# Optimization experiments

Measured on AMD Instinct MI355X. Metric: run time of the kernel, lower is better.

Reference implementation:

```python
import jax, jax.numpy as jnp
import numpy as np

V, MAXLEN, D, I, C, L, S = 32000, 4096, 1024, 4096, 1024, 4, 4096


def setup_inputs() -> dict:
    key = jax.random.key(0)
    ks = jax.random.split(key, 20)
    sd = 0.02
    inp = {
        "input_indices": jax.random.randint(ks[0], (S,), 0, V),
        "emb": jax.random.normal(ks[1], (V, D), jnp.float32) * sd,
        "pos": jax.random.normal(ks[2], (MAXLEN, D), jnp.float32) * sd,
        "Wq": jax.random.normal(ks[3], (L, D, I), jnp.float32) * sd,
        "bq": jnp.zeros((L, I), jnp.float32),
        "Wk": jax.random.normal(ks[4], (L, D, I), jnp.float32) * sd,
        "bk": jnp.zeros((L, I), jnp.float32),
        "Wv": jax.random.normal(ks[5], (L, D, I), jnp.float32) * sd,
        "bv": jnp.zeros((L, I), jnp.float32),
        "Wo": jax.random.normal(ks[6], (L, I, D), jnp.float32) * sd,
        "bo": jnp.zeros((L, D), jnp.float32),
        "W1": jax.random.normal(ks[7], (L, D, I), jnp.float32) * sd,
        "b1": jnp.zeros((L, I), jnp.float32),
        "W2": jax.random.normal(ks[8], (L, I, D), jnp.float32) * sd,
        "b2": jnp.zeros((L, D), jnp.float32),
        "Wout": jax.random.normal(ks[9], (D, C), jnp.float32) * sd,
        "bout": jnp.zeros((C,), jnp.float32),
    }
    return inp


def reference(input_indices, emb, pos, Wq, bq, Wk, bk, Wv, bv, Wo, bo, W1, b1, W2, b2, Wout, bout):
    s = input_indices.shape[0]
    x = emb[input_indices] + pos[:s]  # [S, D]
    causal_mask = jnp.triu(jnp.ones((s, s), bool), k=1)  # True above diagonal -> masked
    scale = 1.0 / np.sqrt(Wq.shape[-1]).astype(np.float32)

    def layer(x, p):
        wq, bq_, wk, bk_, wv, bv_, wo, bo_, w1, b1_, w2, b2_ = p
        q = x @ wq + bq_  # [S, I]
        k = x @ wk + bk_
        v = x @ wv + bv_
        scores = (q @ k.T) * scale  # [S, S]
        scores = jnp.where(causal_mask, -jnp.inf, scores)
        attn = jax.nn.softmax(scores, axis=-1)
        r = x + (attn @ v) @ wo + bo_  # residual + attention output projection
        f = jnp.maximum(r @ w1 + b1_, 0.0) @ w2 + b2_  # ReLU FFN
        return r + f, attn

    x, attention_maps = jax.lax.scan(
        layer, x, (Wq, bq, Wk, bk, Wv, bv, Wo, bo, W1, b1, W2, b2)
    )
    logits = x @ Wout + bout  # [S, C]
    log_probs = jax.nn.log_softmax(logits, axis=-1)
    return log_probs, attention_maps  # [S, C], [L, S, S]
```

## Files before the change

kernel.cpp:

```cpp
#include <hip/hip_runtime.h>
#include <stdint.h>
#include <math.h>

#define S_ 4096
#define D_ 1024
#define I_ 4096
#define C_ 1024
#define L_ 4

typedef unsigned short u16;
typedef short bf16x8 __attribute__((ext_vector_type(8)));
typedef float f32x4 __attribute__((ext_vector_type(4)));

__device__ __forceinline__ u16 f2bf(float f) {
  union { float f; uint32_t u; } c; c.f = f;
  return (u16)((c.u + 0x7FFFu + ((c.u >> 16) & 1u)) >> 16);
}

__device__ __forceinline__ u16 f2h(float f) {
  _Float16 h = (_Float16)f;
  return *(u16*)&h;
}
__device__ __forceinline__ float h2f(u16 b) {
  _Float16 h = *(_Float16*)&b;
  return (float)h;
}

__device__ __forceinline__ void gll16(const void* g, void* l) {
  __builtin_amdgcn_global_load_lds(
      (__attribute__((address_space(1))) void*)(g),
      (__attribute__((address_space(3))) void*)(l), 16, 0, 0);
}

#define BAR() asm volatile("s_barrier" ::: "memory")
#define WAITV(n) asm volatile("s_waitcnt vmcnt(" #n ")" ::: "memory")

__device__ __forceinline__ int xcd_swz(int orig, int nwg) {
  int q8 = nwg >> 3, r8 = nwg & 7;
  int xcd = orig & 7, rem = orig >> 3;
  return (xcd < r8 ? xcd * (q8 + 1) : r8 * (q8 + 1) + (xcd - r8) * q8) + rem;
}

__device__ __forceinline__ void gemm256_body(
    u16* sA, u16* sB,
    const u16* __restrict__ A, const u16* __restrict__ Bt,
    const float* __restrict__ bias, const float* __restrict__ resid,
    float* __restrict__ outF, u16* __restrict__ outB, u16* __restrict__ outH,
    int N, int K, float scale, int relu,
    int row0, int col0, int t0, int t1)
{
  int tid = threadIdx.x, l = tid & 63;
  int w = tid >> 6;
  int wr = w >> 2, wc = w & 3;
  int lrow = l & 15, lq = l >> 4;
  int hb = wc >> 1;
  int rx = lrow & 7;

  const u16* ap[2]; const u16* bp[2]; int dst[2];
#pragma unroll
  for (int u = 0; u < 2; ++u) {
    int c = u * 512 + tid;
    int row = c >> 3;
    int oct = (c & 7) ^ (row & 7);
    ap[u] = A + (size_t)(row0 + row) * K + oct * 8;
    bp[u] = Bt + (size_t)(col0 + row) * K + oct * 8;
    dst[u] = c * 8;
  }

#define STAGE_A(par, hh, t)                                                     \
  { _Pragma("unroll") for (int u = 0; u < 2; ++u)                               \
      gll16(ap[u] + (size_t)(hh) * 128 * K + (t) * 64,                          \
            &sA[((par) * 2 + (hh)) * 8192 + dst[u]]); }
#define STAGE_B(par, hh, t)                                                     \
  { _Pragma("unroll") for (int u = 0; u < 2; ++u)                               \
      gll16(bp[u] + (size_t)(hh) * 128 * K + (t) * 64,                          \
            &sB[((par) * 2 + (hh)) * 8192 + dst[u]]); }
#define LD_A(DST, par, mh)                                                      \
  { _Pragma("unroll") for (int mi = 0; mi < 4; ++mi)                            \
    _Pragma("unroll") for (int kc = 0; kc < 2; ++kc)                            \
      DST[mi][kc] = *(const bf16x8*)&sA[((par) * 2 + wr) * 8192 +               \
          ((mh) * 64 + mi * 16 + lrow) * 64 + (((kc * 4 + lq) ^ rx) * 8)]; }
#define LD_B(DST, par, nh)                                                      \
  { _Pragma("unroll") for (int nj = 0; nj < 2; ++nj)                            \
    _Pragma("unroll") for (int kc = 0; kc < 2; ++kc)                            \
      DST[nj][kc] = *(const bf16x8*)&sB[((par) * 2 + hb) * 8192 +               \
          ((wc & 1) * 64 + (nh) * 32 + nj * 16 + lrow) * 64 +                   \
          (((kc * 4 + lq) ^ rx) * 8)]; }

  f32x4 acc[8][4];
#pragma unroll
  for (int i = 0; i < 8; ++i)
#pragma unroll
    for (int j = 0; j < 4; ++j) {
      acc[i][j][0] = 0.f; acc[i][j][1] = 0.f; acc[i][j][2] = 0.f; acc[i][j][3] = 0.f;
    }

#define MM(AF, MB, NB)                                                          \
  { __builtin_amdgcn_s_setprio(1);                                             \
    _Pragma("unroll") for (int kc = 0; kc < 2; ++kc)                            \
    _Pragma("unroll") for (int mi = 0; mi < 4; ++mi)                            \
    _Pragma("unroll") for (int nj = 0; nj < 2; ++nj)                            \
      acc[(MB) + mi][(NB) + nj] = __builtin_amdgcn_mfma_f32_16x16x32_bf16(      \
          AF[mi][kc], bfv[nj][kc], acc[(MB) + mi][(NB) + nj], 0, 0, 0);         \
    __builtin_amdgcn_s_setprio(0); }

  bf16x8 afA[4][2], afB[4][2], bfv[2][2];

  STAGE_A(0, 0, t0); STAGE_A(0, 1, t0); STAGE_B(0, 0, t0); STAGE_B(0, 1, t0);
  STAGE_A(1, 0, t0 + 1); STAGE_A(1, 1, t0 + 1); STAGE_B(1, 0, t0 + 1);
  WAITV(6);
  BAR();

  for (int t = t0; t < t1; ++t) {
    int p = (t - t0) & 1;
    LD_A(afA, p, 0);
    LD_B(bfv, p, 0);
    LD_A(afB, p, 1);
    if (t + 1 < t1) STAGE_B(p ^ 1, 1, t + 1);
    BAR();
    MM(afA, 0, 0);
    BAR();
    if (t + 2 < t1) STAGE_A(p, 0, t + 2);
    BAR();
    MM(afB, 4, 0);
    BAR();
    LD_B(bfv, p, 1);
    if (t + 2 < t1) STAGE_A(p, 1, t + 2);
    BAR();
    MM(afB, 4, 2);
    BAR();
    if (t + 2 < t1) STAGE_B(p, 0, t + 2);
    BAR();
    MM(afA, 0, 2);
    if (t + 2 < t1) { WAITV(6); } else { WAITV(0); }
    BAR();
  }
#undef STAGE_A
#undef STAGE_B
#undef LD_A
#undef LD_B
#undef MM

  float biasv[4] = {0.f, 0.f, 0.f, 0.f};
  if (bias) {
#pragma unroll
    for (int j = 0; j < 4; ++j) biasv[j] = bias[col0 + wc * 64 + j * 16 + lrow];
  }
#pragma unroll
  for (int i = 0; i < 8; ++i) {
#pragma unroll
    for (int r = 0; r < 4; ++r) {
      int row = row0 + wr * 128 + i * 16 + lq * 4 + r;
      size_t ro = (size_t)row * N;
#pragma unroll
      for (int j = 0; j < 4; ++j) {
        int col = col0 + wc * 64 + j * 16 + lrow;
        float v = acc[i][j][r] * scale + biasv[j];
        if (resid) v += resid[ro + col];
        if (relu) v = fmaxf(v, 0.f);
        if (outF) outF[ro + col] = v;
        if (outB) outB[ro + col] = f2bf(v);
        if (outH) outH[ro + col] = f2h(v);
      }
    }
  }
}

__global__ __launch_bounds__(512, 2) void gemm256k(
    const u16* __restrict__ A, const u16* __restrict__ Bt,
    const float* __restrict__ bias, const float* __restrict__ resid,
    float* __restrict__ outF, u16* __restrict__ outB,
    int M, int N, int K, float scale, int flags, int k0, int k1)
{
  extern __shared__ char smem[];
  int wg = xcd_swz(blockIdx.x, gridDim.x);
  int nbx = N / 256;
  int br = wg / nbx, bc = wg % nbx;
  gemm256_body((u16*)smem, (u16*)smem + 32768, A, Bt, bias, resid, outF, outB,
               nullptr, N, K, scale, flags & 1, br * 256, bc * 256,
               k0 / 64, k1 / 64);
}

struct B3 { const float* b[3]; };
__global__ __launch_bounds__(512, 2) void gemm256_qkv(
    const u16* __restrict__ A, const u16* __restrict__ BtBase,
    B3 b3, u16* __restrict__ outBase, int K)
{
  extern __shared__ char smem[];
  int wg = xcd_swz(blockIdx.x, gridDim.x);
  int z = wg >> 8;
  int tile = wg & 255;
  int br = tile >> 4, bc = tile & 15;
  gemm256_body((u16*)smem, (u16*)smem + 32768, A,
               BtBase + (size_t)z * I_ * D_, b3.b[z], nullptr,
               nullptr, outBase + (size_t)z * S_ * I_, nullptr,
               I_, K, 1.0f, 0, br * 256, bc * 256, 0, K / 64);
}

__global__ __launch_bounds__(512, 2) void gemm256_tri3(
    const u16* __restrict__ A, const u16* __restrict__ Bt,
    u16* __restrict__ out0, u16* __restrict__ out1, u16* __restrict__ out2,
    int K, float scale)
{
  extern __shared__ char smem[];
  int wg = xcd_swz(blockIdx.x, gridDim.x);
  int ntri = gridDim.x / 3;
  int chunk = wg / ntri;
  int tile = wg - chunk * ntri;
  int br = (int)((sqrtf(8.0f * (float)tile + 1.0f) - 1.0f) * 0.5f);
  while ((br + 1) * (br + 2) / 2 <= tile) ++br;
  while (br * (br + 1) / 2 > tile) --br;
  int bc = tile - br * (br + 1) / 2;
  int t0 = (chunk == 0) ? 0 : (chunk == 1 ? 22 : 43);
  int t1 = (chunk == 0) ? 22 : (chunk == 1 ? 43 : 64);
  u16* o = (chunk == 0) ? out0 : (chunk == 1 ? out1 : out2);
  gemm256_body((u16*)smem, (u16*)smem + 32768, A, Bt, nullptr, nullptr,
               nullptr, nullptr, o, S_, K, scale, 0, br * 256, bc * 256, t0, t1);
}

__global__ __launch_bounds__(512, 2) void gemm256_pv(
    const u16* __restrict__ A, const u16* __restrict__ Bt,
    u16* __restrict__ outB, u16* __restrict__ pvH)
{
  extern __shared__ char smem[];
  int wg = xcd_swz(blockIdx.x, gridDim.x);
  if (wg < 128) {
    int br = wg >> 4, bc = wg & 15;
    gemm256_body((u16*)smem, (u16*)smem + 32768, A, Bt, nullptr, nullptr,
                 nullptr, outB, nullptr, I_, S_, 1.0f, 0,
                 br * 256, bc * 256, 0, (br + 1) * 4);
  } else {
    int c = wg - 128;
    int br = 8 + (c >> 5);
    int bc = (c >> 1) & 15;
    int chunk = c & 1;
    int lim = (br + 1) * 4;
    int half = lim >> 1;
    u16* o = pvH + (size_t)chunk * (S_ / 2) * I_ - (size_t)2048 * I_;
    gemm256_body((u16*)smem, (u16*)smem + 32768, A, Bt, nullptr, nullptr,
                 nullptr, nullptr, o, I_, S_, 1.0f, 0,
                 br * 256, bc * 256, chunk ? half : 0, chunk ? lim : half);
  }
}

__global__ __launch_bounds__(256) void combine2pv(
    const u16* __restrict__ pvH, u16* __restrict__ outB)
{
  const int MN = (S_ / 2) * I_;
  int i = (blockIdx.x * 256 + threadIdx.x) * 4;
  ushort4 a = *(const ushort4*)&pvH[i];
  ushort4 b = *(const ushort4*)&pvH[MN + i];
  ushort4 o;
  o.x = f2bf(h2f(a.x) + h2f(b.x));
  o.y = f2bf(h2f(a.y) + h2f(b.y));
  o.z = f2bf(h2f(a.z) + h2f(b.z));
  o.w = f2bf(h2f(a.w) + h2f(b.w));
  *(ushort4*)&outB[(size_t)2048 * I_ + i] = o;
}

__global__ __launch_bounds__(512, 2) void gemm256_ks4(
    const u16* __restrict__ A, const u16* __restrict__ Bt,
    u16* __restrict__ pOut, int M, int N, int K)
{
  extern __shared__ char smem[];
  int wg = xcd_swz(blockIdx.x, gridDim.x);
  int chunk = wg & 3;
  int tile = wg >> 2;
  int nbx = N / 256;
  int br = tile / nbx, bc = tile % nbx;
  u16* o = pOut + (size_t)chunk * M * N;
  int kq = K / 4;
  gemm256_body((u16*)smem, (u16*)smem + 32768, A, Bt, nullptr, nullptr,
               nullptr, nullptr, o, N, K, 1.0f, 0,
               br * 256, bc * 256, (chunk * kq) / 64, ((chunk + 1) * kq) / 64);
}

__global__ __launch_bounds__(256) void combine4(
    const u16* __restrict__ p, const float* __restrict__ bias,
    const float* __restrict__ resid, float* __restrict__ outF,
    u16* __restrict__ outB, int MN, int N)
{
  int i = (blockIdx.x * 256 + threadIdx.x) * 4;
  ushort4 a = *(const ushort4*)&p[i];
  ushort4 b = *(const ushort4*)&p[MN + i];
  ushort4 c = *(const ushort4*)&p[2 * MN + i];
  ushort4 d = *(const ushort4*)&p[3 * MN + i];
  f32x4 v;
  v[0] = h2f(a.x) + h2f(b.x) + h2f(c.x) + h2f(d.x);
  v[1] = h2f(a.y) + h2f(b.y) + h2f(c.y) + h2f(d.y);
  v[2] = h2f(a.z) + h2f(b.z) + h2f(c.z) + h2f(d.z);
  v[3] = h2f(a.w) + h2f(b.w) + h2f(c.w) + h2f(d.w);
  int col = i & (N - 1);
  v += *(const f32x4*)&bias[col];
  v += *(const f32x4*)&resid[i];
  *(f32x4*)&outF[i] = v;
  ushort4 o;
  o.x = f2bf(v[0]); o.y = f2bf(v[1]); o.z = f2bf(v[2]); o.w = f2bf(v[3]);
  *(ushort4*)&outB[i] = o;
}

template <int BM_, int BN_>
__global__ __launch_bounds__(256) void gemm_bt(
    const u16* __restrict__ A, const u16* __restrict__ Bt,
    const float* __restrict__ bias, const float* __restrict__ resid,
    float* __restrict__ outF, u16* __restrict__ outB,
    int M, int N, int K, float scale, int flags)
{
  constexpr int FM = BM_ / 32;
  constexpr int FN = BN_ / 32;
  constexpr int ALOADS = BM_ * 8 / 256;
  constexpr int BLOADS = BN_ * 8 / 256;
  constexpr int WROWS = BM_ / 2;
  constexpr int WCOLS = BN_ / 2;

  int wg = xcd_swz(blockIdx.x, gridDim.x);
  int nbx = N / BN_;
  int br = wg / nbx, bc = wg % nbx;

  int tid = threadIdx.x;
  int l = tid & 63, w = tid >> 6;
  int wr = w >> 1, wc = w & 1;
  int lrow = l & 15, lq = l >> 4;
  int row0 = br * BM_, col0 = bc * BN_;

  __shared__ u16 lA[2][BM_ * 64];
  __shared__ u16 lB[2][BN_ * 64];

  const u16* aptr[ALOADS];
  const u16* bptr[BLOADS];
#pragma unroll
  for (int t = 0; t < ALOADS; ++t) {
    int c = t * 256 + tid;
    int row = c >> 3;
    int oct = (c & 7) ^ (row & 7);
    aptr[t] = A + (size_t)(row0 + row) * K + oct * 8;
  }
#pragma unroll
  for (int t = 0; t < BLOADS; ++t) {
    int c = t * 256 + tid;
    int row = c >> 3;
    int oct = (c & 7) ^ (row & 7);
    bptr[t] = Bt + (size_t)(col0 + row) * K + oct * 8;
  }

#define STAGE(b, koff)                                                          \
  {                                                                             \
    _Pragma("unroll") for (int t = 0; t < ALOADS; ++t)                          \
        gll16(aptr[t] + (koff), &lA[b][(t * 256 + tid) * 8]);                   \
    _Pragma("unroll") for (int t = 0; t < BLOADS; ++t)                          \
        gll16(bptr[t] + (koff), &lB[b][(t * 256 + tid) * 8]);                   \
  }

  f32x4 acc[FM][FN];
#pragma unroll
  for (int i = 0; i < FM; ++i)
#pragma unroll
    for (int j = 0; j < FN; ++j) {
      acc[i][j][0] = 0.f; acc[i][j][1] = 0.f; acc[i][j][2] = 0.f; acc[i][j][3] = 0.f;
    }

  int ktiles = K / 64;
  int rxA = lrow & 7;

  STAGE(0, 0);
  __syncthreads();
  int cur = 0;
  for (int kt = 0; kt < ktiles; ++kt) {
    if (kt + 1 < ktiles) STAGE(cur ^ 1, (kt + 1) * 64);
#pragma unroll
    for (int kc = 0; kc < 2; ++kc) {
      int kq = kc * 4 + lq;
      int octA = (kq ^ rxA) * 8;
      bf16x8 af[FM], bfv[FN];
#pragma unroll
      for (int i = 0; i < FM; ++i)
        af[i] = *(const bf16x8*)&lA[cur][(wr * WROWS + i * 16 + lrow) * 64 + octA];
#pragma unroll
      for (int j = 0; j < FN; ++j)
        bfv[j] = *(const bf16x8*)&lB[cur][(wc * WCOLS + j * 16 + lrow) * 64 + octA];
#pragma unroll
      for (int i = 0; i < FM; ++i)
#pragma unroll
        for (int j = 0; j < FN; ++j)
          acc[i][j] = __builtin_amdgcn_mfma_f32_16x16x32_bf16(af[i], bfv[j], acc[i][j], 0, 0, 0);
    }
    __syncthreads();
    cur ^= 1;
  }
#undef STAGE

  float biasv[FN];
#pragma unroll
  for (int j = 0; j < FN; ++j) biasv[j] = 0.f;
  if (bias) {
#pragma unroll
    for (int j = 0; j < FN; ++j) biasv[j] = bias[col0 + wc * WCOLS + j * 16 + lrow];
  }
  bool do_relu = (flags & 1) != 0;
#pragma unroll
  for (int i = 0; i < FM; ++i) {
#pragma unroll
    for (int r = 0; r < 4; ++r) {
      int row = row0 + wr * WROWS + i * 16 + lq * 4 + r;
      size_t ro = (size_t)row * N;
#pragma unroll
      for (int j = 0; j < FN; ++j) {
        int col = col0 + wc * WCOLS + j * 16 + lrow;
        float v = acc[i][j][r] * scale + biasv[j];
        if (resid) v += resid[ro + col];
        if (do_relu) v = fmaxf(v, 0.f);
        if (outF) outF[ro + col] = v;
        if (outB) outB[ro + col] = f2bf(v);
      }
    }
  }
}

struct T6 {
  const float* src[6];
  u16* dst[6];
};

__global__ __launch_bounds__(256) void trans6_f2b(T6 a) {
  __shared__ float tile[32][33];
  int z = blockIdx.z;
  bool big = (z == 3 || z == 5);
  int R = big ? I_ : D_;
  int C = big ? D_ : I_;
  int bid = blockIdx.y * gridDim.x + blockIdx.x;
  int nbx = C / 32;
  int bx = bid % nbx, by = bid / nbx;
  const float* src = a.src[z];
  u16* dst = a.dst[z];
  int c0 = bx * 32, r0 = by * 32;
  int tx = threadIdx.x & 31, ty = threadIdx.x >> 5;
#pragma unroll
  for (int i = 0; i < 32; i += 8)
    tile[ty + i][tx] = src[(size_t)(r0 + ty + i) * C + c0 + tx];
  __syncthreads();
#pragma unroll
  for (int i = 0; i < 32; i += 8)
    dst[(size_t)(c0 + ty + i) * R + r0 + tx] = f2bf(tile[tx][ty + i]);
}

__global__ __launch_bounds__(256) void trans_f2b(const float* __restrict__ src,
                                                 u16* __restrict__ dst, int R, int C)
{
  __shared__ float tile[32][33];
  int c0 = blockIdx.x * 32, r0 = blockIdx.y * 32;
  int tx = threadIdx.x & 31, ty = threadIdx.x >> 5;
#pragma unroll
  for (int i = 0; i < 32; i += 8)
    tile[ty + i][tx] = src[(size_t)(r0 + ty + i) * C + c0 + tx];
  __syncthreads();
#pragma unroll
  for (int i = 0; i < 32; i += 8)
    dst[(size_t)(c0 + ty + i) * R + r0 + tx] = f2bf(tile[tx][ty + i]);
}

__global__ __launch_bounds__(256) void trans_b2b(const u16* __restrict__ src,
                                                 u16* __restrict__ dst, int R, int C)
{
  __shared__ u16 tile[64][68];
  int c0 = blockIdx.x * 64, r0 = blockIdx.y * 64;
  int tx = threadIdx.x & 63, ty = threadIdx.x >> 6;
#pragma unroll
  for (int i = 0; i < 64; i += 4)
    tile[ty + i][tx] = src[(size_t)(r0 + ty + i) * C + c0 + tx];
  __syncthreads();
#pragma unroll
  for (int i = 0; i < 64; i += 4)
    dst[(size_t)(c0 + ty + i) * R + r0 + tx] = tile[tx][ty + i];
}

__global__ __launch_bounds__(256) void embed_k(const int* __restrict__ idx,
                                               const float* __restrict__ emb,
                                               const float* __restrict__ pos,
                                               float* __restrict__ xf, u16* __restrict__ xb)
{
  int s = blockIdx.y;
  int d = blockIdx.x * 256 + threadIdx.x;
  float v = emb[(size_t)idx[s] * D_ + d] + pos[(size_t)s * D_ + d];
  size_t o = (size_t)s * D_ + d;
  xf[o] = v;
  xb[o] = f2bf(v);
}

__global__ __launch_bounds__(256) void softmax_causal(float* __restrict__ att,
                                                      const u16* __restrict__ p0,
                                                      const u16* __restrict__ p1,
                                                      const u16* __restrict__ p2,
                                                      u16* __restrict__ attB)
{
  int s = blockIdx.x;
  __shared__ float row[S_];
  __shared__ float red[8];
  int tid = threadIdx.x, l = tid & 63, w = tid >> 6;
  int nv = s + 1;
  size_t base = (size_t)s * S_;
  float m = -3.0e38f;
  for (int c = tid; c < nv; c += 256) {
    float v = h2f(p0[base + c]) + h2f(p1[base + c]) + h2f(p2[base + c]);
    row[c] = v; m = fmaxf(m, v);
  }
#pragma unroll
  for (int off = 32; off; off >>= 1) m = fmaxf(m, __shfl_xor(m, off, 64));
  if (l == 0) red[w] = m;
  __syncthreads();
  m = fmaxf(fmaxf(red[0], red[1]), fmaxf(red[2], red[3]));
  float sum = 0.f;
  for (int c = tid; c < nv; c += 256) { float e = __expf(row[c] - m); row[c] = e; sum += e; }
#pragma unroll
  for (int off = 32; off; off >>= 1) sum += __shfl_xor(sum, off, 64);
  if (l == 0) red[4 + w] = sum;
  __syncthreads();
  sum = red[4] + red[5] + red[6] + red[7];
  float inv = 1.0f / sum;
  int nb = ((s >> 8) + 1) * 256;
  for (int c = tid; c < S_; c += 256) {
    float p = (c < nv) ? row[c] * inv : 0.0f;
    att[base + c] = p;
    if (c < nb) attB[base + c] = f2bf(p);
  }
}

__global__ __launch_bounds__(256) void logsoftmax_k(const float* __restrict__ logits,
                                                    float* __restrict__ out)
{
  int s = blockIdx.x;
  int tid = threadIdx.x, l = tid & 63, w = tid >> 6;
  __shared__ float red[8];
  size_t base = (size_t)s * C_;
  float v[4];
  float m = -3.0e38f;
#pragma unroll
  for (int k = 0; k < 4; ++k) { v[k] = logits[base + tid + k * 256]; m = fmaxf(m, v[k]); }
#pragma unroll
  for (int off = 32; off; off >>= 1) m = fmaxf(m, __shfl_xor(m, off, 64));
  if (l == 0) red[w] = m;
  __syncthreads();
  m = fmaxf(fmaxf(red[0], red[1]), fmaxf(red[2], red[3]));
  float sum = 0.f;
#pragma unroll
  for (int k = 0; k < 4; ++k) sum += __expf(v[k] - m);
#pragma unroll
  for (int off = 32; off; off >>= 1) sum += __shfl_xor(sum, off, 64);
  if (l == 0) red[4 + w] = sum;
  __syncthreads();
  sum = red[4] + red[5] + red[6] + red[7];
  float lz = logf(sum);
#pragma unroll
  for (int k = 0; k < 4; ++k) out[base + tid + k * 256] = v[k] - m - lz;
}

extern "C" void kernel_launch(void* const* d_in, const int* in_sizes, int n_in,
                              void* d_out, int out_size, void* d_ws, size_t ws_size,
                              hipStream_t stream) {
  (void)in_sizes; (void)n_in; (void)out_size; (void)ws_size;
  const int*   idx  = (const int*)d_in[0];
  const float* emb  = (const float*)d_in[1];
  const float* pos  = (const float*)d_in[2];
  const float* Wq   = (const float*)d_in[3];
  const float* bq   = (const float*)d_in[4];
  const float* Wk   = (const float*)d_in[5];
  const float* bk   = (const float*)d_in[6];
  const float* Wv   = (const float*)d_in[7];
  const float* bv   = (const float*)d_in[8];
  const float* Wo   = (const float*)d_in[9];
  const float* bo   = (const float*)d_in[10];
  const float* W1   = (const float*)d_in[11];
  const float* b1   = (const float*)d_in[12];
  const float* W2   = (const float*)d_in[13];
  const float* b2   = (const float*)d_in[14];
  const float* Wout = (const float*)d_in[15];
  const float* bout = (const float*)d_in[16];
  float* out = (float*)d_out;

  char* ws = (char*)d_ws;
  const size_t MB = 1024ull * 1024ull;
  float* xres  = (float*)(ws + 0);
  u16*  xbf    = (u16*)(ws + 16 * MB);
  u16*  bufQ   = (u16*)(ws + 24 * MB);
  u16*  bufK   = (u16*)(ws + 56 * MB);
  u16*  bufV   = (u16*)(ws + 88 * MB);
  u16*  bufVT  = (u16*)(ws + 120 * MB);
  u16*  attnB  = (u16*)(ws + 152 * MB);
  float* logit = (float*)(ws + 184 * MB);
  u16* WqT   = (u16*)(ws + 200 * MB);
  u16* WkT   = (u16*)(ws + 208 * MB);
  u16* WvT   = (u16*)(ws + 216 * MB);
  u16* WoT   = (u16*)(ws + 224 * MB);
  u16* W1T   = (u16*)(ws + 232 * MB);
  u16* W2T   = (u16*)(ws + 240 * MB);
  u16* WoutT = (u16*)(ws + 248 * MB);
  u16* attP0 = (u16*)(ws + 256 * MB);
  u16* attP1 = (u16*)(ws + 288 * MB);
  u16* attP2 = (u16*)(ws + 320 * MB);
  u16* shP   = (u16*)(ws + 352 * MB);

  const float iscale = 1.0f / 64.0f;
  const int LDSB = 131072;
  hipFuncSetAttribute((const void*)gemm256k,
                      hipFuncAttributeMaxDynamicSharedMemorySize, LDSB);
  hipFuncSetAttribute((const void*)gemm256_qkv,
                      hipFuncAttributeMaxDynamicSharedMemorySize, LDSB);
  hipFuncSetAttribute((const void*)gemm256_tri3,
                      hipFuncAttributeMaxDynamicSharedMemorySize, LDSB);
  hipFuncSetAttribute((const void*)gemm256_pv,
                      hipFuncAttributeMaxDynamicSharedMemorySize, LDSB);
  hipFuncSetAttribute((const void*)gemm256_ks4,
                      hipFuncAttributeMaxDynamicSharedMemorySize, LDSB);
  const int G_SQ = (S_ / 256) * (I_ / 256);

  embed_k<<<dim3(D_ / 256, S_), 256, 0, stream>>>(idx, emb, pos, xres, xbf);

  for (int layer = 0; layer < L_; ++layer) {
    T6 t6;
    t6.src[0] = Wq + (size_t)layer * D_ * I_; t6.dst[0] = WqT;
    t6.src[1] = Wk + (size_t)layer * D_ * I_; t6.dst[1] = WkT;
    t6.src[2] = Wv + (size_t)layer * D_ * I_; t6.dst[2] = WvT;
    t6.src[3] = Wo + (size_t)layer * I_ * D_; t6.dst[3] = WoT;
    t6.src[4] = W1 + (size_t)layer * D_ * I_; t6.dst[4] = W1T;
    t6.src[5] = W2 + (size_t)layer * I_ * D_; t6.dst[5] = W2T;
    trans6_f2b<<<dim3(128, 32, 6), 256, 0, stream>>>(t6);

    B3 b3;
    b3.b[0] = bq + (size_t)layer * I_;
    b3.b[1] = bk + (size_t)layer * I_;
    b3.b[2] = bv + (size_t)layer * I_;
    gemm256_qkv<<<3 * G_SQ, 512, LDSB, stream>>>(xbf, WqT, b3, bufQ, D_);

    trans_b2b<<<dim3(I_ / 64, S_ / 64), 256, 0, stream>>>(bufV, bufVT, S_, I_);

    float* attL = out + (size_t)S_ * C_ + (size_t)layer * S_ * S_;
    gemm256_tri3<<<3 * 136, 512, LDSB, stream>>>(bufQ, bufK, attP0, attP1, attP2,
                                                 I_, iscale);

    softmax_causal<<<S_, 256, 0, stream>>>(attL, attP0, attP1, attP2, attnB);

    gemm256_pv<<<384, 512, LDSB, stream>>>(attnB, bufVT, bufQ, shP);
    combine2pv<<<(S_ / 2) * (I_ / 1024), 256, 0, stream>>>(shP, bufQ);

    gemm256_ks4<<<(S_ / 256) * (D_ / 256) * 4, 512, LDSB, stream>>>(
        bufQ, WoT, shP, S_, D_, I_);
    combine4<<<(S_ * D_) / 1024, 256, 0, stream>>>(
        shP, bo + (size_t)layer * D_, xres, xres, xbf, S_ * D_, D_);

    gemm256k<<<G_SQ, 512, LDSB, stream>>>(
        xbf, W1T, b1 + (size_t)layer * I_, nullptr, nullptr, bufK,
        S_, I_, D_, 1.0f, 1, 0, D_);

    gemm256_ks4<<<(S_ / 256) * (D_ / 256) * 4, 512, LDSB, stream>>>(
        bufK, W2T, shP, S_, D_, I_);
    combine4<<<(S_ * D_) / 1024, 256, 0, stream>>>(
        shP, b2 + (size_t)layer * D_, xres, xres, xbf, S_ * D_, D_);
  }

  trans_f2b<<<dim3(C_ / 32, D_ / 32), 256, 0, stream>>>(Wout, WoutT, D_, C_);
  gemm_bt<64, 128><<<(S_ / 64) * (C_ / 128), 256, 0, stream>>>(
      xbf, WoutT, bout, nullptr, logit, nullptr, S_, C_, D_, 1.0f, 0);
  logsoftmax_k<<<S_, 256, 0, stream>>>(logit, out);
}
```

Measured before the change: 2.181 ms.

## Write V transposed from QKV GEMM epilogue, widen weight transpose and embed tiles

The QKV GEMM now writes the V projection straight into the transposed layout the PV GEMM needs, staging each half of the output tile through LDS. This removes the separate bf16 transpose kernel and its extra pass over the 32 MB V buffer. The weight transpose kernel moves to 64x64 tiles and the embedding kernel is vectorised to handle 8 elements per thread. The transposed epilogue adds two barriers and an LDS round trip to the V tiles, and its LDS layout with a row pitch of 264 may cause bank conflicts.

Measured after the change: 2.214 ms. About the same (+1.5%).

```diff
diff --git a/kernel.cpp b/kernel.cpp
--- a/kernel.cpp
+++ b/kernel.cpp
@@ -46,6 +46,7 @@
     const u16* __restrict__ A, const u16* __restrict__ Bt,
     const float* __restrict__ bias, const float* __restrict__ resid,
     float* __restrict__ outF, u16* __restrict__ outB, u16* __restrict__ outH,
+    u16* __restrict__ outT, int ldT,
     int N, int K, float scale, int relu,
     int row0, int col0, int t0, int t1)
 {
@@ -146,6 +147,37 @@
 #pragma unroll
     for (int j = 0; j < 4; ++j) biasv[j] = bias[col0 + wc * 64 + j * 16 + lrow];
   }
+
+  if (outT) {
+    u16* tlds = sA;
+    int myhalf = wc >> 1;
+#pragma unroll
+    for (int half = 0; half < 2; ++half) {
+      BAR();
+      if (myhalf == half) {
+#pragma unroll
+        for (int i = 0; i < 8; ++i)
+#pragma unroll
+          for (int r = 0; r < 4; ++r)
+#pragma unroll
+            for (int j = 0; j < 4; ++j) {
+              int cl = (wc * 64 + j * 16 + lrow) & 127;
+              int rowl = wr * 128 + i * 16 + lq * 4 + r;
+              tlds[cl * 264 + rowl] = f2bf(acc[i][j][r] + biasv[j]);
+            }
+      }
+      BAR();
+      int cl = tid >> 2, seg = tid & 3;
+      size_t gb = (size_t)(col0 + half * 128 + cl) * ldT + row0 + seg * 64;
+#pragma unroll
+      for (int r8 = 0; r8 < 64; r8 += 8) {
+        bf16x8 v = *(const bf16x8*)&tlds[cl * 264 + seg * 64 + r8];
+        *(bf16x8*)&outT[gb + r8] = v;
+      }
+    }
+    return;
+  }
+
 #pragma unroll
   for (int i = 0; i < 8; ++i) {
 #pragma unroll
@@ -177,24 +209,31 @@
   int nbx = N / 256;
   int br = wg / nbx, bc = wg % nbx;
   gemm256_body((u16*)smem, (u16*)smem + 32768, A, Bt, bias, resid, outF, outB,
-               nullptr, N, K, scale, flags & 1, br * 256, bc * 256,
+               nullptr, nullptr, 0, N, K, scale, flags & 1, br * 256, bc * 256,
                k0 / 64, k1 / 64);
 }
 
 struct B3 { const float* b[3]; };
 __global__ __launch_bounds__(512, 2) void gemm256_qkv(
     const u16* __restrict__ A, const u16* __restrict__ BtBase,
-    B3 b3, u16* __restrict__ outBase, int K)
+    B3 b3, u16* __restrict__ outQK, u16* __restrict__ vT, int K)
 {
   extern __shared__ char smem[];
   int wg = xcd_swz(blockIdx.x, gridDim.x);
   int z = wg >> 8;
   int tile = wg & 255;
   int br = tile >> 4, bc = tile & 15;
-  gemm256_body((u16*)smem, (u16*)smem + 32768, A,
-               BtBase + (size_t)z * I_ * D_, b3.b[z], nullptr,
-               nullptr, outBase + (size_t)z * S_ * I_, nullptr,
-               I_, K, 1.0f, 0, br * 256, bc * 256, 0, K / 64);
+  if (z < 2) {
+    gemm256_body((u16*)smem, (u16*)smem + 32768, A,
+                 BtBase + (size_t)z * I_ * D_, b3.b[z], nullptr,
+                 nullptr, outQK + (size_t)z * S_ * I_, nullptr, nullptr, 0,
+                 I_, K, 1.0f, 0, br * 256, bc * 256, 0, K / 64);
+  } else {
+    gemm256_body((u16*)smem, (u16*)smem + 32768, A,
+                 BtBase + (size_t)2 * I_ * D_, b3.b[2], nullptr,
+                 nullptr, nullptr, nullptr, vT, S_,
+                 I_, K, 1.0f, 0, br * 256, bc * 256, 0, K / 64);
+  }
 }
 
 __global__ __launch_bounds__(512, 2) void gemm256_tri3(
@@ -215,7 +254,8 @@
   int t1 = (chunk == 0) ? 22 : (chunk == 1 ? 43 : 64);
   u16* o = (chunk == 0) ? out0 : (chunk == 1 ? out1 : out2);
   gemm256_body((u16*)smem, (u16*)smem + 32768, A, Bt, nullptr, nullptr,
-               nullptr, nullptr, o, S_, K, scale, 0, br * 256, bc * 256, t0, t1);
+               nullptr, nullptr, o, nullptr, 0,
+               S_, K, scale, 0, br * 256, bc * 256, t0, t1);
 }
 
 __global__ __launch_bounds__(512, 2) void gemm256_pv(
@@ -227,7 +267,7 @@
   if (wg < 128) {
     int br = wg >> 4, bc = wg & 15;
     gemm256_body((u16*)smem, (u16*)smem + 32768, A, Bt, nullptr, nullptr,
-                 nullptr, outB, nullptr, I_, S_, 1.0f, 0,
+                 nullptr, outB, nullptr, nullptr, 0, I_, S_, 1.0f, 0,
                  br * 256, bc * 256, 0, (br + 1) * 4);
   } else {
     int c = wg - 128;
@@ -238,7 +278,7 @@
     int half = lim >> 1;
     u16* o = pvH + (size_t)chunk * (S_ / 2) * I_ - (size_t)2048 * I_;
     gemm256_body((u16*)smem, (u16*)smem + 32768, A, Bt, nullptr, nullptr,
-                 nullptr, nullptr, o, I_, S_, 1.0f, 0,
+                 nullptr, nullptr, o, nullptr, 0, I_, S_, 1.0f, 0,
                  br * 256, bc * 256, chunk ? half : 0, chunk ? lim : half);
   }
 }
@@ -271,7 +311,7 @@
   u16* o = pOut + (size_t)chunk * M * N;
   int kq = K / 4;
   gemm256_body((u16*)smem, (u16*)smem + 32768, A, Bt, nullptr, nullptr,
-               nullptr, nullptr, o, N, K, 1.0f, 0,
+               nullptr, nullptr, o, nullptr, 0, N, K, 1.0f, 0,
                br * 256, bc * 256, (chunk * kq) / 64, ((chunk + 1) * kq) / 64);
 }
 
@@ -422,17 +462,32 @@
 };
 
 __global__ __launch_bounds__(256) void trans6_f2b(T6 a) {
-  __shared__ float tile[32][33];
+  __shared__ float tile[64][65];
   int z = blockIdx.z;
   bool big = (z == 3 || z == 5);
   int R = big ? I_ : D_;
   int C = big ? D_ : I_;
   int bid = blockIdx.y * gridDim.x + blockIdx.x;
-  int nbx = C / 32;
+  int nbx = C / 64;
   int bx = bid % nbx, by = bid / nbx;
   const float* src = a.src[z];
   u16* dst = a.dst[z];
-  int c0 = bx * 32, r0 = by * 32;
+  int c0 = bx * 64, r0 = by * 64;
+  int tx = threadIdx.x & 63, ty = threadIdx.x >> 6;
+#pragma unroll
+  for (int i = 0; i < 64; i += 4)
+    tile[ty + i][tx] = src[(size_t)(r0 + ty + i) * C + c0 + tx];
+  __syncthreads();
+#pragma unroll
+  for (int i = 0; i < 64; i += 4)
+    dst[(size_t)(c0 + ty + i) * R + r0 + tx] = f2bf(tile[tx][ty + i]);
+}
+
+__global__ __launch_bounds__(256) void trans_f2b(const float* __restrict__ src,
+                                                 u16* __restrict__ dst, int R, int C)
+{
+  __shared__ float tile[32][33];
+  int c0 = blockIdx.x * 32, r0 = blockIdx.y * 32;
   int tx = threadIdx.x & 31, ty = threadIdx.x >> 5;
 #pragma unroll
   for (int i = 0; i < 32; i += 8)
@@ -441,36 +496,6 @@
 #pragma unroll
   for (int i = 0; i < 32; i += 8)
     dst[(size_t)(c0 + ty + i) * R + r0 + tx] = f2bf(tile[tx][ty + i]);
-}
-
-__global__ __launch_bounds__(256) void trans_f2b(const float* __restrict__ src,
-                                                 u16* __restrict__ dst, int R, int C)
-{
-  __shared__ float tile[32][33];
-  int c0 = blockIdx.x * 32, r0 = blockIdx.y * 32;
-  int tx = threadIdx.x & 31, ty = threadIdx.x >> 5;
-#pragma unroll
-  for (int i = 0; i < 32; i += 8)
-    tile[ty + i][tx] = src[(size_t)(r0 + ty + i) * C + c0 + tx];
-  __syncthreads();
-#pragma unroll
-  for (int i = 0; i < 32; i += 8)
-    dst[(size_t)(c0 + ty + i) * R + r0 + tx] = f2bf(tile[tx][ty + i]);
-}
-
-__global__ __launch_bounds__(256) void trans_b2b(const u16* __restrict__ src,
-                                                 u16* __restrict__ dst, int R, int C)
-{
-  __shared__ u16 tile[64][68];
-  int c0 = blockIdx.x * 64, r0 = blockIdx.y * 64;
-  int tx = threadIdx.x & 63, ty = threadIdx.x >> 6;
-#pragma unroll
-  for (int i = 0; i < 64; i += 4)
-    tile[ty + i][tx] = src[(size_t)(r0 + ty + i) * C + c0 + tx];
-  __syncthreads();
-#pragma unroll
-  for (int i = 0; i < 64; i += 4)
-    dst[(size_t)(c0 + ty + i) * R + r0 + tx] = tile[tx][ty + i];
 }
 
 __global__ __launch_bounds__(256) void embed_k(const int* __restrict__ idx,
@@ -478,12 +503,20 @@
                                                const float* __restrict__ pos,
                                                float* __restrict__ xf, u16* __restrict__ xb)
 {
-  int s = blockIdx.y;
-  int d = blockIdx.x * 256 + threadIdx.x;
-  float v = emb[(size_t)idx[s] * D_ + d] + pos[(size_t)s * D_ + d];
-  size_t o = (size_t)s * D_ + d;
-  xf[o] = v;
-  xb[o] = f2bf(v);
+  int i = (blockIdx.x * 256 + threadIdx.x) * 8;
+  int s = i >> 10;
+  int d = i & (D_ - 1);
+  const float* e = emb + (size_t)idx[s] * D_ + d;
+  const float* p = pos + (size_t)s * D_ + d;
+  f32x4 v0 = *(const f32x4*)e + *(const f32x4*)p;
+  f32x4 v1 = *(const f32x4*)(e + 4) + *(const f32x4*)(p + 4);
+  *(f32x4*)&xf[i] = v0;
+  *(f32x4*)&xf[i + 4] = v1;
+  ushort4 b0, b1;
+  b0.x = f2bf(v0[0]); b0.y = f2bf(v0[1]); b0.z = f2bf(v0[2]); b0.w = f2bf(v0[3]);
+  b1.x = f2bf(v1[0]); b1.y = f2bf(v1[1]); b1.z = f2bf(v1[2]); b1.w = f2bf(v1[3]);
+  *(ushort4*)&xb[i] = b0;
+  *(ushort4*)&xb[i + 4] = b1;
 }
 
 __global__ __launch_bounds__(256) void softmax_causal(float* __restrict__ att,
@@ -582,7 +615,6 @@
   u16*  xbf    = (u16*)(ws + 16 * MB);
   u16*  bufQ   = (u16*)(ws + 24 * MB);
   u16*  bufK   = (u16*)(ws + 56 * MB);
-  u16*  bufV   = (u16*)(ws + 88 * MB);
   u16*  bufVT  = (u16*)(ws + 120 * MB);
   u16*  attnB  = (u16*)(ws + 152 * MB);
   float* logit = (float*)(ws + 184 * MB);
@@ -612,7 +644,7 @@
                       hipFuncAttributeMaxDynamicSharedMemorySize, LDSB);
   const int G_SQ = (S_ / 256) * (I_ / 256);
 
-  embed_k<<<dim3(D_ / 256, S_), 256, 0, stream>>>(idx, emb, pos, xres, xbf);
+  embed_k<<<(S_ * D_) / (256 * 8), 256, 0, stream>>>(idx, emb, pos, xres, xbf);
 
   for (int layer = 0; layer < L_; ++layer) {
     T6 t6;
@@ -622,15 +654,13 @@
     t6.src[3] = Wo + (size_t)layer * I_ * D_; t6.dst[3] = WoT;
     t6.src[4] = W1 + (size_t)layer * D_ * I_; t6.dst[4] = W1T;
     t6.src[5] = W2 + (size_t)layer * I_ * D_; t6.dst[5] = W2T;
-    trans6_f2b<<<dim3(128, 32, 6), 256, 0, stream>>>(t6);
+    trans6_f2b<<<dim3(64, 16, 6), 256, 0, stream>>>(t6);
 
     B3 b3;
     b3.b[0] = bq + (size_t)layer * I_;
     b3.b[1] = bk + (size_t)layer * I_;
     b3.b[2] = bv + (size_t)layer * I_;
-    gemm256_qkv<<<3 * G_SQ, 512, LDSB, stream>>>(xbf, WqT, b3, bufQ, D_);
-
-    trans_b2b<<<dim3(I_ / 64, S_ / 64), 256, 0, stream>>>(bufV, bufVT, S_, I_);
+    gemm256_qkv<<<3 * G_SQ, 512, LDSB, stream>>>(xbf, WqT, b3, bufQ, bufVT, D_);
 
     float* attL = out + (size_t)S_ * C_ + (size_t)layer * S_ * S_;
     gemm256_tri3<<<3 * 136, 512, LDSB, stream>>>(bufQ, bufK, attP0, attP1, attP2,
```
